# Performance work log

Hardware: AMD Instinct MI355X
Metric: run time of the kernel (lower is better)

## Reference

```python
import jax, jax.numpy as jnp
import numpy as np
import math

D_POLY = 2  # polynomial order d
N_NODES = 50000
IN_FEATS = 128
H_FEATS = 64
N_EDGES = 800000


def calc_thetas(d):
    # Beta-wavelet polynomial coefficients (ascending order), matching calculate_theta2
    thetas = []
    for i in range(d + 1):
        p = np.poly1d([1.0])
        for _ in range(i):
            p = p * np.poly1d([0.5, 0.0])      # (x/2)
        for _ in range(d - i):
            p = p * np.poly1d([-0.5, 1.0])     # (1 - x/2)
        beta = math.gamma(i + 1) * math.gamma(d + 1 - i) / math.gamma(d + 2)
        p = p / beta
        asc = p.coeffs[::-1]                   # ascending coefficients
        asc = np.concatenate([asc, np.zeros(d + 1 - len(asc))])
        thetas.append(asc.astype(np.float32))
    return thetas

THETAS = calc_thetas(D_POLY)


def setup_inputs() -> dict:
    key = jax.random.key(0)
    ks = jax.random.split(key, 7)
    features = jax.random.normal(ks[0], (N_NODES, IN_FEATS), dtype=jnp.float32)
    src = jax.random.randint(ks[1], (N_EDGES,), 0, N_NODES)
    dst = jax.random.randint(ks[2], (N_EDGES,), 0, N_NODES)
    s1 = 1.0 / math.sqrt(IN_FEATS)
    W1 = jax.random.uniform(ks[3], (H_FEATS, IN_FEATS), jnp.float32, -s1, s1)
    b1 = jnp.zeros((H_FEATS,), jnp.float32)
    s2 = 1.0 / math.sqrt(H_FEATS * (D_POLY + 1))
    W2 = jax.random.uniform(ks[4], (H_FEATS, H_FEATS * (D_POLY + 1)), jnp.float32, -s2, s2)
    b2 = jnp.zeros((H_FEATS,), jnp.float32)
    return {"features": features, "src": src, "dst": dst,
            "W1": W1, "b1": b1, "W2": W2, "b2": b2}


def reference(features, src, dst, W1, b1, W2, b2):
    N = features.shape[0]
    # linear1 + ReLU
    x = jax.nn.relu(features @ W1.T + b1)  # [N, H]
    # D^{-1/2} from in-degrees (clamped at 1)
    deg = jax.ops.segment_sum(jnp.ones_like(dst, dtype=x.dtype), dst, num_segments=N)
    D_invsqrt = jnp.clip(deg, 1.0, None) ** -0.5  # [N]
    D_invsqrt = D_invsqrt[:, None]

    def unn_laplacian(f):
        # f - D^{-1/2} A D^{-1/2} f   (aggregation onto destination nodes)
        agg = jax.ops.segment_sum((f * D_invsqrt)[src], dst, num_segments=N)
        return f - agg * D_invsqrt

    outs = []
    for theta in THETAS:
        f = x
        h = theta[0] * x
        for k in range(1, len(theta)):
            f = unn_laplacian(f)
            h = h + theta[k] * f
        outs.append(h)
    feats_final = jnp.concatenate(outs, axis=-1)  # [N, H*(d+1)]
    return feats_final @ W2.T + b2
```

## Files before the change

### kernel.cpp

```cpp
#include <hip/hip_runtime.h>

#define NN 50000
#define NE 800000
#define INF 128
#define HF 64
#define K2 192
#define MAXDEG 64

typedef __attribute__((ext_vector_type(8))) short short8;
typedef __attribute__((ext_vector_type(4))) float float4v;

__device__ inline unsigned short f2bf(float x) {
    unsigned int u = __float_as_uint(x);
    u += 0x7FFFu + ((u >> 16) & 1u);
    return (unsigned short)(u >> 16);
}
__device__ inline float bf2f(unsigned short h) {
    return __uint_as_float(((unsigned int)h) << 16);
}
__device__ inline float bflo(unsigned int p) { return __uint_as_float(p << 16); }
__device__ inline float bfhi(unsigned int p) { return __uint_as_float(p & 0xFFFF0000u); }


__global__ __launch_bounds__(256) void fill_ell_part(const int* __restrict__ src,
                                                     const int* __restrict__ dst,
                                                     int* __restrict__ cnt,
                                                     int* __restrict__ ell) {
    int chunk = blockIdx.x >> 3;
    int p     = blockIdx.x & 7;
    int e = chunk * 256 + threadIdx.x;
    if (e >= NE) return;
    int d = dst[e];
    if (d / 6250 != p) return;
    int pos = atomicAdd(&cnt[d], 1);
    if (pos < MAXDEG) ell[d * MAXDEG + pos] = src[e];
}

__global__ void dinv_kernel(int* __restrict__ cnt, float* __restrict__ dinv) {
    int i = blockIdx.x * blockDim.x + threadIdx.x;
    if (i < NN) {
        int c = cnt[i];
        if (c > MAXDEG) c = MAXDEG;
        cnt[i] = c;
        dinv[i] = rsqrtf((float)(c < 1 ? 1 : c));
    }
}


__global__ void pack_b(const float* __restrict__ W1, const float* __restrict__ W2,
                       unsigned short* __restrict__ Bp1, unsigned short* __restrict__ Bp2) {
    int gid = blockIdx.x * 256 + threadIdx.x;
    if (gid >= 20480) return;
    if (gid < 8192) {
        int j  = gid & 7;
        int l  = (gid >> 3) & 63;
        int nt = (gid >> 9) & 3;
        int kc = gid >> 11;
        int n = nt * 16 + (l & 15);
        int k = kc * 32 + (l >> 4) * 8 + j;
        Bp1[gid] = f2bf(W1[n * INF + k]);
    } else {
        int g = gid - 8192;
        int j  = g & 7;
        int l  = (g >> 3) & 63;
        int nt = (g >> 9) & 3;
        int kc = g >> 11;
        int n = nt * 16 + (l & 15);
        int k = kc * 32 + (l >> 4) * 8 + j;
        const float* row = W2 + (size_t)n * K2;
        float v;
        if (k < 64) {
            v = 3.0f * row[k];
        } else if (k < 128) {
            int c = k - 64;
            v = -3.0f * row[c] + 3.0f * row[64 + c];
        } else {
            int c = k - 128;
            v = 0.75f * row[c] - 1.5f * row[64 + c] + 0.75f * row[128 + c];
        }
        Bp2[g] = f2bf(v);
    }
}


__global__ __launch_bounds__(256) void gemm1_mfma(const float* __restrict__ F,
                                                  const unsigned short* __restrict__ Bp,
                                                  const float* __restrict__ b1,
                                                  const float* __restrict__ dinv,
                                                  unsigned short* __restrict__ xb,
                                                  unsigned short* __restrict__ hb0) {
    int tid  = threadIdx.x;
    int lane = tid & 63;
    int wv   = tid >> 6;
    int m0   = blockIdx.x * 64 + wv * 16;
    if (m0 >= NN) return;
    int mrow = lane & 15;
    int q    = lane >> 4;

    float4v acc[4];
#pragma unroll
    for (int nt = 0; nt < 4; ++nt) acc[nt] = (float4v){0.f, 0.f, 0.f, 0.f};

    const float* arow = F + (size_t)(m0 + mrow) * INF + q * 8;
#pragma unroll
    for (int kc = 0; kc < INF / 32; ++kc) {
        const float* ap = arow + kc * 32;
        float4v a0 = *reinterpret_cast<const float4v*>(ap);
        float4v a1 = *reinterpret_cast<const float4v*>(ap + 4);
        short8 af;
        af[0] = (short)f2bf(a0[0]); af[1] = (short)f2bf(a0[1]);
        af[2] = (short)f2bf(a0[2]); af[3] = (short)f2bf(a0[3]);
        af[4] = (short)f2bf(a1[0]); af[5] = (short)f2bf(a1[1]);
        af[6] = (short)f2bf(a1[2]); af[7] = (short)f2bf(a1[3]);
#pragma unroll
        for (int nt = 0; nt < 4; ++nt) {
            short8 bf = *reinterpret_cast<const short8*>(Bp + (((kc * 4 + nt) * 64 + lane) << 3));
            acc[nt] = __builtin_amdgcn_mfma_f32_16x16x32_bf16(af, bf, acc[nt], 0, 0, 0);
        }
    }

    float dn[4];
#pragma unroll
    for (int r = 0; r < 4; ++r) dn[r] = dinv[m0 + q * 4 + r];

#pragma unroll
    for (int nt = 0; nt < 4; ++nt) {
        int n = nt * 16 + mrow;
        float bv = b1[n];
#pragma unroll
        for (int r = 0; r < 4; ++r) {
            int node = m0 + q * 4 + r;
            float v = acc[nt][r] + bv;
            v = v > 0.0f ? v : 0.0f;
            xb [(size_t)node * HF + n] = f2bf(v);
            hb0[(size_t)node * HF + n] = f2bf(v * dn[r]);
        }
    }
}


template <bool WRITE_H>
__global__ __launch_bounds__(256) void gather_pair(const int* __restrict__ ell,
                                                   const int* __restrict__ cnt,
                                                   const float* __restrict__ dinv,
                                                   const unsigned short* __restrict__ fin,
                                                   const unsigned short* __restrict__ hb,
                                                   unsigned short* __restrict__ fout,
                                                   unsigned short* __restrict__ hout) {
    int lane  = threadIdx.x & 63;
    int wv    = threadIdx.x >> 6;
    int which = lane >> 5;
    int jj    = lane & 31;
    int n = blockIdx.x * 8 + wv * 2 + which;
    if (n >= NN) return;
    int deg = cnt[n];

    int sv0 = 0, sv1 = 0;
    if (jj < deg)      sv0 = ell[n * MAXDEG + jj];
    if (jj + 32 < deg) sv1 = ell[n * MAXDEG + 32 + jj];

    const unsigned int* hbd = (const unsigned int*)hb;
    int base = which * 32;

    float ax0 = 0.f, ay0 = 0.f, ax1 = 0.f, ay1 = 0.f;
    float ax2 = 0.f, ay2 = 0.f, ax3 = 0.f, ay3 = 0.f;

    int d0 = deg < 32 ? deg : 32;
    int k = 0;
    for (; k + 3 < d0; k += 4) {
        int s0 = __shfl(sv0, base + k);
        int s1 = __shfl(sv0, base + k + 1);
        int s2 = __shfl(sv0, base + k + 2);
        int s3 = __shfl(sv0, base + k + 3);
        unsigned int p0 = hbd[(size_t)s0 * 32 + jj];
        unsigned int p1 = hbd[(size_t)s1 * 32 + jj];
        unsigned int p2 = hbd[(size_t)s2 * 32 + jj];
        unsigned int p3 = hbd[(size_t)s3 * 32 + jj];
        ax0 += bflo(p0); ay0 += bfhi(p0);
        ax1 += bflo(p1); ay1 += bfhi(p1);
        ax2 += bflo(p2); ay2 += bfhi(p2);
        ax3 += bflo(p3); ay3 += bfhi(p3);
    }
    for (; k < d0; ++k) {
        unsigned int p = hbd[(size_t)__shfl(sv0, base + k) * 32 + jj];
        ax0 += bflo(p); ay0 += bfhi(p);
    }
    k = 32;
    for (; k + 3 < deg; k += 4) {
        int s0 = __shfl(sv1, base + (k & 31));
        int s1 = __shfl(sv1, base + ((k + 1) & 31));
        int s2 = __shfl(sv1, base + ((k + 2) & 31));
        int s3 = __shfl(sv1, base + ((k + 3) & 31));
        unsigned int p0 = hbd[(size_t)s0 * 32 + jj];
        unsigned int p1 = hbd[(size_t)s1 * 32 + jj];
        unsigned int p2 = hbd[(size_t)s2 * 32 + jj];
        unsigned int p3 = hbd[(size_t)s3 * 32 + jj];
        ax0 += bflo(p0); ay0 += bfhi(p0);
        ax1 += bflo(p1); ay1 += bfhi(p1);
        ax2 += bflo(p2); ay2 += bfhi(p2);
        ax3 += bflo(p3); ay3 += bfhi(p3);
    }
    for (; k < deg; ++k) {
        unsigned int p = hbd[(size_t)__shfl(sv1, base + (k & 31)) * 32 + jj];
        ax0 += bflo(p); ay0 += bfhi(p);
    }

    float accx = (ax0 + ax1) + (ax2 + ax3);
    float accy = (ay0 + ay1) + (ay2 + ay3);
    float dn = dinv[n];

    unsigned int xv = ((const unsigned int*)fin)[(size_t)n * 32 + jj];
    float fx = bflo(xv) - accx * dn;
    float fy = bfhi(xv) - accy * dn;
    ((unsigned int*)fout)[(size_t)n * 32 + jj] =
        (unsigned int)f2bf(fx) | ((unsigned int)f2bf(fy) << 16);
    if (WRITE_H) {
        ((unsigned int*)hout)[(size_t)n * 32 + jj] =
            (unsigned int)f2bf(fx * dn) | ((unsigned int)f2bf(fy * dn) << 16);
    }
}


__global__ __launch_bounds__(256) void gemm2_mfma(const unsigned short* __restrict__ xb,
                                                  const unsigned short* __restrict__ f1b,
                                                  const unsigned short* __restrict__ f2b,
                                                  const unsigned short* __restrict__ Bp,
                                                  const float* __restrict__ b2,
                                                  float* __restrict__ out) {
    int tid  = threadIdx.x;
    int lane = tid & 63;
    int wv   = tid >> 6;
    int m0   = blockIdx.x * 64 + wv * 16;
    if (m0 >= NN) return;
    int mrow = lane & 15;
    int q    = lane >> 4;

    float4v acc[4];
#pragma unroll
    for (int nt = 0; nt < 4; ++nt) acc[nt] = (float4v){0.f, 0.f, 0.f, 0.f};

    const unsigned short* ax = xb  + (size_t)(m0 + mrow) * HF + q * 8;
    const unsigned short* a1 = f1b + (size_t)(m0 + mrow) * HF + q * 8;
    const unsigned short* a2 = f2b + (size_t)(m0 + mrow) * HF + q * 8;

#pragma unroll
    for (int kc = 0; kc < 6; ++kc) {
        short8 af;
        if (kc < 2)      af = *reinterpret_cast<const short8*>(ax + kc * 32);
        else if (kc < 4) af = *reinterpret_cast<const short8*>(a1 + (kc - 2) * 32);
        else             af = *reinterpret_cast<const short8*>(a2 + (kc - 4) * 32);
#pragma unroll
        for (int nt = 0; nt < 4; ++nt) {
            short8 bf = *reinterpret_cast<const short8*>(Bp + (((kc * 4 + nt) * 64 + lane) << 3));
            acc[nt] = __builtin_amdgcn_mfma_f32_16x16x32_bf16(af, bf, acc[nt], 0, 0, 0);
        }
    }

#pragma unroll
    for (int nt = 0; nt < 4; ++nt) {
        int n = nt * 16 + mrow;
        float bv = b2[n];
#pragma unroll
        for (int r = 0; r < 4; ++r) {
            int node = m0 + q * 4 + r;
            out[(size_t)node * HF + n] = acc[nt][r] + bv;
        }
    }
}


extern "C" void kernel_launch(void* const* d_in, const int* in_sizes, int n_in,
                              void* d_out, int out_size, void* d_ws, size_t ws_size,
                              hipStream_t stream) {
    const float* features = (const float*)d_in[0];
    const int*   src      = (const int*)d_in[1];
    const int*   dst      = (const int*)d_in[2];
    const float* W1       = (const float*)d_in[3];
    const float* b1       = (const float*)d_in[4];
    const float* W2       = (const float*)d_in[5];
    const float* b2       = (const float*)d_in[6];
    float* out = (float*)d_out;

    unsigned short* xb  = (unsigned short*)d_ws;
    unsigned short* hb0 = xb  + (size_t)NN * HF;
    unsigned short* f1b = hb0 + (size_t)NN * HF;
    unsigned short* hb1 = f1b + (size_t)NN * HF;
    unsigned short* f2b = hb1 + (size_t)NN * HF;
    unsigned short* Bp1 = f2b + (size_t)NN * HF;
    unsigned short* Bp2 = Bp1 + 8192;
    int*   ell  = (int*)(Bp2 + 12288);
    int*   cnt  = ell + (size_t)NN * MAXDEG;
    float* dinv = (float*)(cnt + NN);

    hipMemsetAsync(cnt, 0, NN * sizeof(int), stream);

    fill_ell_part<<<((NE + 255) / 256) * 8, 256, 0, stream>>>(src, dst, cnt, ell);
    dinv_kernel<<<(NN + 255) / 256, 256, 0, stream>>>(cnt, dinv);

    pack_b<<<80, 256, 0, stream>>>(W1, W2, Bp1, Bp2);

    gemm1_mfma<<<(NN + 63) / 64, 256, 0, stream>>>(features, Bp1, b1, dinv, xb, hb0);

    gather_pair<true ><<<(NN + 7) / 8, 256, 0, stream>>>(ell, cnt, dinv, xb,  hb0, f1b, hb1);
    gather_pair<false><<<(NN + 7) / 8, 256, 0, stream>>>(ell, cnt, dinv, f1b, hb1, f2b, nullptr);

    gemm2_mfma<<<(NN + 63) / 64, 256, 0, stream>>>(xb, f1b, f2b, Bp2, b2, out);
}
```

Baseline: 178.0 us.

## Use 16-bit ELL indices and four nodes per wave in gather with zero-row padding

Stores ELL neighbor indices as 16-bit values and rewrites the gather so each 16-lane group handles one node, loading 8-byte chunks (four bf16 features) per lane. Out-of-range slots point to a zero padding row, which removes the per-node tail loops and lets the wave loop run to the maximum degree of its four nodes. The aim is less index traffic and fewer, wider loads per neighbor. The cost is extra zero-row loads when degrees differ within a wave. Casting src to unsigned short truncates node ids at or above 65536; with 50000 nodes that limit is not reached.

```diff
diff --git a/kernel.cpp b/kernel.cpp
--- a/kernel.cpp
+++ b/kernel.cpp
@@ -9,6 +9,8 @@
 
 typedef __attribute__((ext_vector_type(8))) short short8;
 typedef __attribute__((ext_vector_type(4))) float float4v;
+typedef __attribute__((ext_vector_type(4))) unsigned short ushort4v;
+typedef __attribute__((ext_vector_type(2))) unsigned int uint2v;
 
 __device__ inline unsigned short f2bf(float x) {
     unsigned int u = __float_as_uint(x);
@@ -25,7 +27,7 @@
 __global__ __launch_bounds__(256) void fill_ell_part(const int* __restrict__ src,
                                                      const int* __restrict__ dst,
                                                      int* __restrict__ cnt,
-                                                     int* __restrict__ ell) {
+                                                     unsigned short* __restrict__ ell) {
     int chunk = blockIdx.x >> 3;
     int p     = blockIdx.x & 7;
     int e = chunk * 256 + threadIdx.x;
@@ -33,16 +35,22 @@
     int d = dst[e];
     if (d / 6250 != p) return;
     int pos = atomicAdd(&cnt[d], 1);
-    if (pos < MAXDEG) ell[d * MAXDEG + pos] = src[e];
-}
-
-__global__ void dinv_kernel(int* __restrict__ cnt, float* __restrict__ dinv) {
+    if (pos < MAXDEG) ell[d * MAXDEG + pos] = (unsigned short)src[e];
+}
+
+__global__ void dinv_kernel(int* __restrict__ cnt, float* __restrict__ dinv,
+                            unsigned short* __restrict__ hb0,
+                            unsigned short* __restrict__ hb1) {
     int i = blockIdx.x * blockDim.x + threadIdx.x;
     if (i < NN) {
         int c = cnt[i];
         if (c > MAXDEG) c = MAXDEG;
         cnt[i] = c;
         dinv[i] = rsqrtf((float)(c < 1 ? 1 : c));
+    }
+    if (i < HF) {
+        hb0[(size_t)NN * HF + i] = 0;
+        hb1[(size_t)NN * HF + i] = 0;
     }
 }
 
@@ -140,7 +148,7 @@
 
 
 template <bool WRITE_H>
-__global__ __launch_bounds__(256) void gather_pair(const int* __restrict__ ell,
+__global__ __launch_bounds__(256) void gather_quad(const unsigned short* __restrict__ ell,
                                                    const int* __restrict__ cnt,
                                                    const float* __restrict__ dinv,
                                                    const unsigned short* __restrict__ fin,
@@ -149,74 +157,63 @@
                                                    unsigned short* __restrict__ hout) {
     int lane  = threadIdx.x & 63;
     int wv    = threadIdx.x >> 6;
-    int which = lane >> 5;
-    int jj    = lane & 31;
-    int n = blockIdx.x * 8 + wv * 2 + which;
-    if (n >= NN) return;
+    int which = lane >> 4;
+    int jj    = lane & 15;
+    int n = blockIdx.x * 16 + wv * 4 + which;
     int deg = cnt[n];
 
-    int sv0 = 0, sv1 = 0;
-    if (jj < deg)      sv0 = ell[n * MAXDEG + jj];
-    if (jj + 32 < deg) sv1 = ell[n * MAXDEG + 32 + jj];
-
-    const unsigned int* hbd = (const unsigned int*)hb;
-    int base = which * 32;
-
-    float ax0 = 0.f, ay0 = 0.f, ax1 = 0.f, ay1 = 0.f;
-    float ax2 = 0.f, ay2 = 0.f, ax3 = 0.f, ay3 = 0.f;
-
-    int d0 = deg < 32 ? deg : 32;
-    int k = 0;
-    for (; k + 3 < d0; k += 4) {
-        int s0 = __shfl(sv0, base + k);
-        int s1 = __shfl(sv0, base + k + 1);
-        int s2 = __shfl(sv0, base + k + 2);
-        int s3 = __shfl(sv0, base + k + 3);
-        unsigned int p0 = hbd[(size_t)s0 * 32 + jj];
-        unsigned int p1 = hbd[(size_t)s1 * 32 + jj];
-        unsigned int p2 = hbd[(size_t)s2 * 32 + jj];
-        unsigned int p3 = hbd[(size_t)s3 * 32 + jj];
-        ax0 += bflo(p0); ay0 += bfhi(p0);
-        ax1 += bflo(p1); ay1 += bfhi(p1);
-        ax2 += bflo(p2); ay2 += bfhi(p2);
-        ax3 += bflo(p3); ay3 += bfhi(p3);
-    }
-    for (; k < d0; ++k) {
-        unsigned int p = hbd[(size_t)__shfl(sv0, base + k) * 32 + jj];
-        ax0 += bflo(p); ay0 += bfhi(p);
-    }
-    k = 32;
-    for (; k + 3 < deg; k += 4) {
-        int s0 = __shfl(sv1, base + (k & 31));
-        int s1 = __shfl(sv1, base + ((k + 1) & 31));
-        int s2 = __shfl(sv1, base + ((k + 2) & 31));
-        int s3 = __shfl(sv1, base + ((k + 3) & 31));
-        unsigned int p0 = hbd[(size_t)s0 * 32 + jj];
-        unsigned int p1 = hbd[(size_t)s1 * 32 + jj];
-        unsigned int p2 = hbd[(size_t)s2 * 32 + jj];
-        unsigned int p3 = hbd[(size_t)s3 * 32 + jj];
-        ax0 += bflo(p0); ay0 += bfhi(p0);
-        ax1 += bflo(p1); ay1 += bfhi(p1);
-        ax2 += bflo(p2); ay2 += bfhi(p2);
-        ax3 += bflo(p3); ay3 += bfhi(p3);
-    }
-    for (; k < deg; ++k) {
-        unsigned int p = hbd[(size_t)__shfl(sv1, base + (k & 31)) * 32 + jj];
-        ax0 += bflo(p); ay0 += bfhi(p);
-    }
-
-    float accx = (ax0 + ax1) + (ax2 + ax3);
-    float accy = (ay0 + ay1) + (ay2 + ay3);
+    ushort4v ids = *reinterpret_cast<const ushort4v*>(ell + (size_t)n * MAXDEG + jj * 4);
+    int slot = jj * 4;
+    int s0 = (slot + 0 < deg) ? (int)ids[0] : NN;
+    int s1 = (slot + 1 < deg) ? (int)ids[1] : NN;
+    int s2 = (slot + 2 < deg) ? (int)ids[2] : NN;
+    int s3 = (slot + 3 < deg) ? (int)ids[3] : NN;
+
+    int wmax = deg;
+    wmax = max(wmax, __shfl_xor(wmax, 16));
+    wmax = max(wmax, __shfl_xor(wmax, 32));
+
+    const uint2v* hbd = (const uint2v*)hb;
+    int base = which * 16;
+
+    float a0=0,a1=0,a2=0,a3=0;
+    float b0=0,b1=0,b2=0,b3=0;
+    float c0=0,c1=0,c2=0,c3=0;
+    float d0=0,d1=0,d2=0,d3=0;
+
+    for (int k = 0; k < wmax; k += 4) {
+        int o = base + (k >> 2);
+        int t0 = __shfl(s0, o), t1 = __shfl(s1, o);
+        int t2 = __shfl(s2, o), t3 = __shfl(s3, o);
+        uint2v p0 = hbd[(size_t)t0 * 16 + jj];
+        uint2v p1 = hbd[(size_t)t1 * 16 + jj];
+        uint2v p2 = hbd[(size_t)t2 * 16 + jj];
+        uint2v p3 = hbd[(size_t)t3 * 16 + jj];
+        a0 += bflo(p0[0]); a1 += bfhi(p0[0]); a2 += bflo(p0[1]); a3 += bfhi(p0[1]);
+        b0 += bflo(p1[0]); b1 += bfhi(p1[0]); b2 += bflo(p1[1]); b3 += bfhi(p1[1]);
+        c0 += bflo(p2[0]); c1 += bfhi(p2[0]); c2 += bflo(p2[1]); c3 += bfhi(p2[1]);
+        d0 += bflo(p3[0]); d1 += bfhi(p3[0]); d2 += bflo(p3[1]); d3 += bfhi(p3[1]);
+    }
+    float e0 = (a0 + b0) + (c0 + d0);
+    float e1 = (a1 + b1) + (c1 + d1);
+    float e2 = (a2 + b2) + (c2 + d2);
+    float e3 = (a3 + b3) + (c3 + d3);
     float dn = dinv[n];
 
-    unsigned int xv = ((const unsigned int*)fin)[(size_t)n * 32 + jj];
-    float fx = bflo(xv) - accx * dn;
-    float fy = bfhi(xv) - accy * dn;
-    ((unsigned int*)fout)[(size_t)n * 32 + jj] =
-        (unsigned int)f2bf(fx) | ((unsigned int)f2bf(fy) << 16);
+    uint2v xv = ((const uint2v*)fin)[(size_t)n * 16 + jj];
+    float f0 = bflo(xv[0]) - e0 * dn;
+    float f1 = bfhi(xv[0]) - e1 * dn;
+    float f2 = bflo(xv[1]) - e2 * dn;
+    float f3 = bfhi(xv[1]) - e3 * dn;
+    uint2v ov;
+    ov[0] = (unsigned int)f2bf(f0) | ((unsigned int)f2bf(f1) << 16);
+    ov[1] = (unsigned int)f2bf(f2) | ((unsigned int)f2bf(f3) << 16);
+    ((uint2v*)fout)[(size_t)n * 16 + jj] = ov;
     if (WRITE_H) {
-        ((unsigned int*)hout)[(size_t)n * 32 + jj] =
-            (unsigned int)f2bf(fx * dn) | ((unsigned int)f2bf(fy * dn) << 16);
+        uint2v hv;
+        hv[0] = (unsigned int)f2bf(f0 * dn) | ((unsigned int)f2bf(f1 * dn) << 16);
+        hv[1] = (unsigned int)f2bf(f2 * dn) | ((unsigned int)f2bf(f3 * dn) << 16);
+        ((uint2v*)hout)[(size_t)n * 16 + jj] = hv;
     }
 }
 
@@ -283,26 +280,26 @@
 
     unsigned short* xb  = (unsigned short*)d_ws;
     unsigned short* hb0 = xb  + (size_t)NN * HF;
-    unsigned short* f1b = hb0 + (size_t)NN * HF;
+    unsigned short* f1b = hb0 + (size_t)(NN + 1) * HF;
     unsigned short* hb1 = f1b + (size_t)NN * HF;
-    unsigned short* f2b = hb1 + (size_t)NN * HF;
+    unsigned short* f2b = hb1 + (size_t)(NN + 1) * HF;
     unsigned short* Bp1 = f2b + (size_t)NN * HF;
     unsigned short* Bp2 = Bp1 + 8192;
-    int*   ell  = (int*)(Bp2 + 12288);
-    int*   cnt  = ell + (size_t)NN * MAXDEG;
+    unsigned short* ell = Bp2 + 12288;
+    int*   cnt  = (int*)(ell + (size_t)NN * MAXDEG);
     float* dinv = (float*)(cnt + NN);
 
     hipMemsetAsync(cnt, 0, NN * sizeof(int), stream);
 
     fill_ell_part<<<((NE + 255) / 256) * 8, 256, 0, stream>>>(src, dst, cnt, ell);
-    dinv_kernel<<<(NN + 255) / 256, 256, 0, stream>>>(cnt, dinv);
+    dinv_kernel<<<(NN + 255) / 256, 256, 0, stream>>>(cnt, dinv, hb0, hb1);
 
     pack_b<<<80, 256, 0, stream>>>(W1, W2, Bp1, Bp2);
 
     gemm1_mfma<<<(NN + 63) / 64, 256, 0, stream>>>(features, Bp1, b1, dinv, xb, hb0);
 
-    gather_pair<true ><<<(NN + 7) / 8, 256, 0, stream>>>(ell, cnt, dinv, xb,  hb0, f1b, hb1);
-    gather_pair<false><<<(NN + 7) / 8, 256, 0, stream>>>(ell, cnt, dinv, f1b, hb1, f2b, nullptr);
+    gather_quad<true ><<<NN / 16, 256, 0, stream>>>(ell, cnt, dinv, xb,  hb0, f1b, hb1);
+    gather_quad<false><<<NN / 16, 256, 0, stream>>>(ell, cnt, dinv, f1b, hb1, f2b, nullptr);
 
     gemm2_mfma<<<(NN + 63) / 64, 256, 0, stream>>>(xb, f1b, f2b, Bp2, b2, out);
 }
```

Result: faster. 172.8 us (-2.9%).
